# Performance work log

Hardware: AMD Instinct MI355X
Metric: run time of the kernel (lower is better)

## Reference

```python
import math
import jax
import jax.numpy as jnp
import numpy as np

GRID = 12  # distance + 1 for distance-11 surface code


def _ln(x, s, b):
    m = jnp.mean(x, axis=-1, keepdims=True)
    v = jnp.mean((x - m) ** 2, axis=-1, keepdims=True)
    return (x - m) / jnp.sqrt(v + 1e-5) * s + b


def _gelu(x):
    return jax.nn.gelu(x, approximate=False)  # torch F.gelu default = exact erf


def _forward(meas, event, leak, event_leak, bias, pm_w, pm_b, pe_w, pe_b, pl_w, pl_b, pel_w, pel_b,
             stab_emb, cyc_emb, er_ln_s, er_ln_b, er_fc1_w, er_fc1_b, er_fc2_w, er_fc2_b,
             ln1_s, ln1_b, Wb, Wq, bq, Wk, bk, Wv, bv, Wo, bo, ln2_s, ln2_b,
             f1_w, f1_b, f2_w, f2_b, conv_w, conv_b, lnf_s, lnf_b,
             P, sc_w, sc_b, dr_w, dr_b, rb1_w, rb1_b, rb2_w, rb2_b, out_w, out_b,
             stab_ids, cycle_ids):
    B, T, S = meas.shape
    L, Hh, _, da = Wq.shape
    dm = Wv.shape[-1]
    d = P.shape[0]

    # per-head additive attention bias, identical across cycles: (L,B,H,S,S)
    Bp = jnp.einsum('bijd,ldh->lbhij', bias, Wb)
    scale = 1.0 / jnp.sqrt(jnp.asarray(da, meas.dtype))
    pos_emb = stab_emb[stab_ids]  # (S, d)

    def embed(t):
        h = (meas[:, t, :, None] * pm_w + pm_b
             + event[:, t, :, None] * pe_w + pe_b
             + leak[:, t, :, None] * pl_w + pl_b
             + event_leak[:, t, :, None] * pel_w + pel_b
             + pos_emb[None] + cyc_emb[cycle_ids[t]][None, None, :])
        for r in range(er_fc1_w.shape[0]):
            hn = _ln(h, er_ln_s[r], er_ln_b[r])
            h = h + jnp.matmul(_gelu(jnp.matmul(hn, er_fc1_w[r]) + er_fc1_b[r]), er_fc2_w[r]) + er_fc2_b[r]
        return h

    X = jnp.zeros((B, S, d), meas.dtype)
    for t in range(T):  # recurrent application of RNNCore over cycles
        X = (X + embed(t)) / jnp.sqrt(jnp.asarray(2.0, meas.dtype))
        for l in range(L):
            Xn = _ln(X, ln1_s[l], ln1_b[l])
            Q = jnp.einsum('bsd,hde->bhse', Xn, Wq[l]) + bq[l][None, :, None, :]
            Kt = jnp.einsum('bsd,hde->bhse', Xn, Wk[l]) + bk[l][None, :, None, :]
            V = jnp.einsum('bsd,hdm->bhsm', Xn, Wv[l]) + bv[l][None, :, None, :]
            Sc = jnp.einsum('bhqe,bhke->bhqk', Q, Kt) + Bp[l]  # bias added BEFORE 1/sqrt(da)
            A = jax.nn.softmax(Sc * scale, axis=-1)
            O = jnp.einsum('bhqk,bhkm->bhqm', A, V)
            Y = O.transpose(0, 2, 1, 3).reshape(B, S, Hh * dm)
            X = X + jnp.matmul(Y, Wo[l]) + bo[l]
            Xn = _ln(X, ln2_s[l], ln2_b[l])
            Yf = jnp.matmul(Xn, f1_w[l]) + f1_b[l]
            a, g = jnp.split(Yf, 2, axis=-1)
            X = X + jnp.matmul(_gelu(a) * g, f2_w[l]) + f2_b[l]
            # conv block: residual depth-mixing Conv1d(k=3, SAME) over the stabilizer axis
            xc = jnp.transpose(X, (0, 2, 1))  # (B, d, S)
            c = jax.lax.conv_general_dilated(xc, conv_w[l], (1,), 'SAME',
                                             dimension_numbers=('NCH', 'OIH', 'NCH'))
            X = X + _gelu(jnp.transpose(c + conv_b[l][None, :, None], (0, 2, 1)))

    # readout
    Xn = _ln(X, lnf_s, lnf_b)
    pad = jnp.broadcast_to(P, (B, GRID * GRID - S, d))  # empty grid cells filled with P
    grid = jnp.concatenate([Xn, pad], axis=1).reshape(B, GRID, GRID, d).transpose(0, 3, 1, 2)
    x = jax.lax.conv_general_dilated(grid, sc_w, (2, 2), 'VALID',
                                     dimension_numbers=('NCHW', 'OIHW', 'NCHW')) + sc_b[None, :, None, None]
    x = _gelu(x)
    x = jnp.einsum('bdhw,rd->brhw', x, dr_w) + dr_b[None, :, None, None]
    x = _gelu(x)
    x = x.mean(axis=2)  # basis 'z': pool over grid rows -> (B, rd, K)
    Kk = x.shape[2]
    x = x.transpose(0, 2, 1).reshape(B * Kk, -1)
    for r in range(rb1_w.shape[0]):
        x = x + jnp.matmul(_gelu(jnp.matmul(x, rb1_w[r]) + rb1_b[r]), rb2_w[r]) + rb2_b[r]
    logits = (jnp.matmul(x, out_w) + out_b).reshape(B, Kk).mean(axis=1)
    return logits


def setup_inputs() -> dict:
    key = jax.random.key(0)
    ks = iter(jax.random.split(key, 100))

    def rn(shape, s=0.02):
        return (s * jax.random.normal(next(ks), shape)).astype(jnp.float32)

    B, T, S, d = 16, 8, 120, 128
    L, H, da, dm, db = 2, 4, 32, 32, 32
    rd, nrb, ncyc = 48, 16, 32
    z = lambda *sh: jnp.zeros(sh, jnp.float32)
    o = lambda *sh: jnp.ones(sh, jnp.float32)
    inp = {
        'meas': jax.random.uniform(next(ks), (B, T, S), jnp.float32),
        'event': jax.random.uniform(next(ks), (B, T, S), jnp.float32),
        'leak': jax.random.uniform(next(ks), (B, T, S), jnp.float32),
        'event_leak': jax.random.uniform(next(ks), (B, T, S), jnp.float32),
        'bias': rn((B, S, S, db), 0.5),
        'pm_w': rn((d,)), 'pm_b': z(d),
        'pe_w': rn((d,)), 'pe_b': z(d),
        'pl_w': rn((d,)), 'pl_b': z(d),
        'pel_w': rn((d,)), 'pel_b': z(d),
        'stab_emb': rn((S, d)),
        'cyc_emb': rn((ncyc, d)),
        'er_ln_s': o(2, d), 'er_ln_b': z(2, d),
        'er_fc1_w': rn((2, d, d)), 'er_fc1_b': z(2, d),
        'er_fc2_w': rn((2, d, d)), 'er_fc2_b': z(2, d),
        'ln1_s': o(L, d), 'ln1_b': z(L, d),
        'Wb': rn((L, db, H)),
        'Wq': rn((L, H, d, da)), 'bq': z(L, H, da),
        'Wk': rn((L, H, d, da)), 'bk': z(L, H, da),
        'Wv': rn((L, H, d, dm)), 'bv': z(L, H, dm),
        'Wo': rn((L, H * dm, d)), 'bo': z(L, d),
        'ln2_s': o(L, d), 'ln2_b': z(L, d),
        'f1_w': rn((L, d, 4 * d)), 'f1_b': z(L, 4 * d),
        'f2_w': rn((L, 2 * d, d)), 'f2_b': z(L, d),
        'conv_w': rn((L, d, d, 3)), 'conv_b': z(L, d),
        'lnf_s': o(d), 'lnf_b': z(d),
        'P': z(d),
        'sc_w': rn((d, d, 2, 2)), 'sc_b': z(d),
        'dr_w': rn((rd, d)), 'dr_b': z(rd),
        'rb1_w': rn((nrb, rd, rd)), 'rb1_b': z(nrb, rd),
        'rb2_w': rn((nrb, rd, rd)), 'rb2_b': z(nrb, rd),
        'out_w': rn((rd,)), 'out_b': z(),
        'stab_ids': jnp.arange(S, dtype=jnp.int32),
        'cycle_ids': jnp.arange(T, dtype=jnp.int32),
    }
    return inp


def reference(meas, event, leak, event_leak, bias, pm_w, pm_b, pe_w, pe_b, pl_w, pl_b, pel_w, pel_b,
              stab_emb, cyc_emb, er_ln_s, er_ln_b, er_fc1_w, er_fc1_b, er_fc2_w, er_fc2_b,
              ln1_s, ln1_b, Wb, Wq, bq, Wk, bk, Wv, bv, Wo, bo, ln2_s, ln2_b,
              f1_w, f1_b, f2_w, f2_b, conv_w, conv_b, lnf_s, lnf_b,
              P, sc_w, sc_b, dr_w, dr_b, rb1_w, rb1_b, rb2_w, rb2_b, out_w, out_b,
              stab_ids, cycle_ids):
    return _forward(meas, event, leak, event_leak, bias, pm_w, pm_b, pe_w, pe_b, pl_w, pl_b, pel_w, pel_b,
                    stab_emb, cyc_emb, er_ln_s, er_ln_b, er_fc1_w, er_fc1_b, er_fc2_w, er_fc2_b,
                    ln1_s, ln1_b, Wb, Wq, bq, Wk, bk, Wv, bv, Wo, bo, ln2_s, ln2_b,
                    f1_w, f1_b, f2_w, f2_b, conv_w, conv_b, lnf_s, lnf_b,
                    P, sc_w, sc_b, dr_w, dr_b, rb1_w, rb1_b, rb2_w, rb2_b, out_w, out_b,
                    stab_ids, cycle_ids)
```

## Files before the change

kernel.cpp:

```cpp
#include <hip/hip_runtime.h>
#include <math.h>

#define Dm 128
#define Ssz 120
#define Bsz 16
#define Tcy 8
#define Hh 4
#define DA 32
#define Lly 2
#define RT 8
#define NRT ((Bsz*Ssz)/RT)
#define NROW (Bsz*Ssz)

struct KParams {
    const float *meas, *event_, *leak, *event_leak, *bias;
    const float *pm_w, *pm_b, *pe_w, *pe_b, *pl_w, *pl_b, *pel_w, *pel_b;
    const float *stab_emb, *cyc_emb;
    const float *er_ln_s, *er_ln_b, *er_fc1_w, *er_fc1_b, *er_fc2_w, *er_fc2_b;
    const float *ln1_s, *ln1_b, *Wb, *Wq, *bq, *Wk, *bk, *Wv, *bv, *Wo, *bo;
    const float *ln2_s, *ln2_b, *f1_w, *f1_b, *f2_w, *f2_b, *conv_w, *conv_b;
    const float *lnf_s, *lnf_b, *Pp, *sc_w, *sc_b, *dr_w, *dr_b;
    const float *rb1_w, *rb1_b, *rb2_w, *rb2_b, *out_w, *out_b;
    const int *stab_ids, *cycle_ids;
    float *Bp, *Q, *K, *V, *Y2, *cwT, *E;
};

__device__ __forceinline__ float gelu_f(float x) {
    return 0.5f * x * (1.0f + erff(x * 0.70710678118654752f));
}

__device__ __forceinline__ int swz16(int i, int per_b) {
    return ((((i & 7) << 1) | ((i >> 3) & 1)) * per_b) + (i >> 4);
}

__device__ __forceinline__ void ln_rows8(const float (*src)[Dm], float (*dst)[Dm],
                                         const float* sg, const float* bg, int tid) {
    int r = tid >> 6, g = tid & 63;
    float x0 = src[r][g], x1 = src[r][g + 64];
    float s1 = x0 + x1;
#pragma unroll
    for (int off = 32; off; off >>= 1) s1 += __shfl_xor(s1, off);
    float m = s1 * (1.f / 128.f);
    float d0 = x0 - m, d1 = x1 - m;
    float s2 = d0 * d0 + d1 * d1;
#pragma unroll
    for (int off = 32; off; off >>= 1) s2 += __shfl_xor(s2, off);
    float rstd = rsqrtf(s2 * (1.f / 128.f) + 1e-5f);
    dst[r][g]      = d0 * rstd * sg[g]      + bg[g];
    dst[r][g + 64] = d1 * rstd * sg[g + 64] + bg[g + 64];
}

__device__ __forceinline__ void ln32(const float (*src)[Dm], float (*dst)[Dm],
                                     const float* sg, const float* bg, int tid) {
    int r = tid >> 4, g = tid & 15;
    float v[8];
    float s1 = 0.f;
#pragma unroll
    for (int k = 0; k < 8; k++) { v[k] = src[r][g + 16 * k]; s1 += v[k]; }
#pragma unroll
    for (int off = 8; off; off >>= 1) s1 += __shfl_xor(s1, off);
    float m = s1 * (1.f / 128.f);
    float s2 = 0.f;
#pragma unroll
    for (int k = 0; k < 8; k++) { float d = v[k] - m; s2 += d * d; }
#pragma unroll
    for (int off = 8; off; off >>= 1) s2 += __shfl_xor(s2, off);
    float rstd = rsqrtf(s2 * (1.f / 128.f) + 1e-5f);
#pragma unroll
    for (int k = 0; k < 8; k++)
        dst[r][g + 16 * k] = (v[k] - m) * rstd * sg[g + 16 * k] + bg[g + 16 * k];
}

__global__ __launch_bounds__(256) void k_prepcw(KParams p) {
    int idx = blockIdx.x * 256 + threadIdx.x;
    if (idx >= Lly * Dm * 3 * Dm) return;
    int o = idx & 127; int rest = idx >> 7;
    int k = rest % 3; rest /= 3;
    int i = rest & 127; int l = rest >> 7;
    p.cwT[idx] = p.conv_w[((l * Dm + o) * Dm + i) * 3 + k];
}

__global__ __launch_bounds__(128) void k_bias(KParams p) {
    int blk = blockIdx.x;
    int b = blk / Ssz, i = blk % Ssz;
    int j = threadIdx.x;
    if (j >= Ssz) return;
    const float4* br4 = (const float4*)(p.bias + ((size_t)(b * Ssz + i) * Ssz + j) * 32);
    float a[Lly][4];
#pragma unroll
    for (int l = 0; l < Lly; l++)
#pragma unroll
        for (int h = 0; h < 4; h++) a[l][h] = 0.f;
#pragma unroll
    for (int c4 = 0; c4 < 8; c4++) {
        float bv[4]; *(float4*)bv = br4[c4];
#pragma unroll
        for (int u = 0; u < 4; u++) {
#pragma unroll
            for (int l = 0; l < Lly; l++) {
                const float* w = p.Wb + (l * 32 + c4 * 4 + u) * Hh;
                a[l][0] += bv[u] * w[0]; a[l][1] += bv[u] * w[1];
                a[l][2] += bv[u] * w[2]; a[l][3] += bv[u] * w[3];
            }
        }
    }
    size_t hs = (size_t)Ssz * Ssz;
#pragma unroll
    for (int l = 0; l < Lly; l++) {
        size_t base = (((size_t)(l * Bsz + b) * Hh) * Ssz + i) * Ssz + j;
        p.Bp[base] = a[l][0]; p.Bp[base + hs] = a[l][1];
        p.Bp[base + 2 * hs] = a[l][2]; p.Bp[base + 3 * hs] = a[l][3];
    }
}

__global__ __launch_bounds__(512) void k_embed_all(KParams p) {
    __shared__ float h[32][Dm], hn[32][Dm], t1[32][Dm];
    int t = blockIdx.x / 60, tile = blockIdx.x % 60;
    int row0 = tile * 32;
    int tid = threadIdx.x;
    int cid = p.cycle_ids[t];
    for (int idx = tid; idx < 32 * Dm; idx += 512) {
        int r = idx >> 7, j = idx & 127;
        int row = row0 + r;
        int b = row / Ssz, s = row % Ssz;
        int sid = p.stab_ids[s];
        int mi = (b * Tcy + t) * Ssz + s;
        h[r][j] = p.meas[mi] * p.pm_w[j] + p.pm_b[j]
                + p.event_[mi] * p.pe_w[j] + p.pe_b[j]
                + p.leak[mi] * p.pl_w[j] + p.pl_b[j]
                + p.event_leak[mi] * p.pel_w[j] + p.pel_b[j]
                + p.stab_emb[sid * Dm + j] + p.cyc_emb[cid * Dm + j];
    }
    __syncthreads();
    int g2 = tid >> 7, j = tid & 127;
    for (int rbk = 0; rbk < 2; rbk++) {
        ln32(h, hn, p.er_ln_s + rbk * Dm, p.er_ln_b + rbk * Dm, tid);
        __syncthreads();
        const float* W1 = p.er_fc1_w + rbk * Dm * Dm;
        float acc[8];
#pragma unroll
        for (int rr = 0; rr < 8; rr++) acc[rr] = 0.f;
#pragma unroll 2
        for (int i4 = 0; i4 < 32; i4++) {
            float4 xv[8];
#pragma unroll
            for (int rr = 0; rr < 8; rr++) xv[rr] = *(const float4*)&hn[8 * g2 + rr][i4 * 4];
#pragma unroll
            for (int u = 0; u < 4; u++) {
                float w = W1[(i4 * 4 + u) * Dm + j];
#pragma unroll
                for (int rr = 0; rr < 8; rr++) acc[rr] += ((const float*)&xv[rr])[u] * w;
            }
        }
        float b1 = p.er_fc1_b[rbk * Dm + j];
#pragma unroll
        for (int rr = 0; rr < 8; rr++) t1[8 * g2 + rr][j] = gelu_f(acc[rr] + b1);
        __syncthreads();
        const float* W2 = p.er_fc2_w + rbk * Dm * Dm;
#pragma unroll
        for (int rr = 0; rr < 8; rr++) acc[rr] = 0.f;
#pragma unroll 2
        for (int i4 = 0; i4 < 32; i4++) {
            float4 xv[8];
#pragma unroll
            for (int rr = 0; rr < 8; rr++) xv[rr] = *(const float4*)&t1[8 * g2 + rr][i4 * 4];
#pragma unroll
            for (int u = 0; u < 4; u++) {
                float w = W2[(i4 * 4 + u) * Dm + j];
#pragma unroll
                for (int rr = 0; rr < 8; rr++) acc[rr] += ((const float*)&xv[rr])[u] * w;
            }
        }
        float b2 = p.er_fc2_b[rbk * Dm + j];
#pragma unroll
        for (int rr = 0; rr < 8; rr++) h[8 * g2 + rr][j] += acc[rr] + b2;
        __syncthreads();
    }
    for (int idx = tid; idx < 32 * Dm; idx += 512) {
        int r = idx >> 7, jj = idx & 127;
        p.E[((size_t)t * NROW + row0 + r) * Dm + jj] = h[r][jj];
    }
}

__global__ __launch_bounds__(512) void k_a(KParams p, const float* Xprev, float* Xcur,
                                           int l, int t, int doConv) {
    __shared__ float xr[RT + 2][Dm];
    __shared__ float xn[RT][Dm];
    int rb = swz16(blockIdx.x, Ssz / RT);
    int row0 = rb * RT;
    int b = row0 / Ssz, s0 = row0 % Ssz;
    int tid = threadIdx.x;
    const float inv = 0.70710678118654752f;
    int g2 = tid >> 7, j = tid & 127;

    if (doConv) {
        int lconv = l ^ 1;
        {
            float4* xr4 = (float4*)&xr[0][0];
            for (int i = tid; i < (RT + 2) * Dm / 4; i += 512) {
                int rr = i >> 5, c = i & 31;
                int s = s0 + rr - 1;
                float4 v = make_float4(0.f, 0.f, 0.f, 0.f);
                if (s >= 0 && s < Ssz) v = *(const float4*)(Xprev + (b * Ssz + s) * Dm + 4 * c);
                xr4[i] = v;
            }
        }
        __syncthreads();
        const float* CW = p.cwT + (size_t)lconv * Dm * 3 * Dm + j;
        float a0 = 0.f, a1 = 0.f;
#pragma unroll 2
        for (int i4 = 0; i4 < 32; i4++) {
            float4 xv[4];
#pragma unroll
            for (int rr = 0; rr < 4; rr++) xv[rr] = *(const float4*)&xr[2 * g2 + rr][i4 * 4];
#pragma unroll
            for (int u = 0; u < 4; u++) {
                int i = i4 * 4 + u;
                float w0 = CW[(i * 3 + 0) * Dm];
                float w1 = CW[(i * 3 + 1) * Dm];
                float w2 = CW[(i * 3 + 2) * Dm];
                a0 += w0 * ((const float*)&xv[0])[u] + w1 * ((const float*)&xv[1])[u] + w2 * ((const float*)&xv[2])[u];
                a1 += w0 * ((const float*)&xv[1])[u] + w1 * ((const float*)&xv[2])[u] + w2 * ((const float*)&xv[3])[u];
            }
        }
        float cb = p.conv_b[lconv * Dm + j];
        float v0 = xr[2 * g2 + 1][j] + gelu_f(a0 + cb);
        float v1 = xr[2 * g2 + 2][j] + gelu_f(a1 + cb);
        if (l == 0) {
            v0 = (v0 + p.E[((size_t)t * NROW + row0 + 2 * g2) * Dm + j]) * inv;
            v1 = (v1 + p.E[((size_t)t * NROW + row0 + 2 * g2 + 1) * Dm + j]) * inv;
        }
        Xcur[(row0 + 2 * g2) * Dm + j]     = v0;
        Xcur[(row0 + 2 * g2 + 1) * Dm + j] = v1;
        xn[2 * g2][j] = v0; xn[2 * g2 + 1][j] = v1;
    } else {
        float v0 = p.E[(size_t)(row0 + 2 * g2) * Dm + j] * inv;
        float v1 = p.E[(size_t)(row0 + 2 * g2 + 1) * Dm + j] * inv;
        Xcur[(row0 + 2 * g2) * Dm + j]     = v0;
        Xcur[(row0 + 2 * g2 + 1) * Dm + j] = v1;
        xn[2 * g2][j] = v0; xn[2 * g2 + 1][j] = v1;
    }
    __syncthreads();
    ln_rows8(xn, xn, p.ln1_s + l * Dm, p.ln1_b + l * Dm, tid);
    __syncthreads();
    if (tid < 384) {
        int out = tid >> 7, col = tid & 127;
        int h = col >> 5, e = col & 31;
        const float* W = (out == 0 ? p.Wq : out == 1 ? p.Wk : p.Wv)
                       + ((size_t)(l * Hh + h) * Dm) * DA + e;
        const float* bbp = (out == 0 ? p.bq : out == 1 ? p.bk : p.bv) + (l * Hh + h) * DA + e;
        float acc[8];
#pragma unroll
        for (int rr = 0; rr < 8; rr++) acc[rr] = 0.f;
#pragma unroll 2
        for (int i4 = 0; i4 < 32; i4++) {
            float4 xv[8];
#pragma unroll
            for (int rr = 0; rr < 8; rr++) xv[rr] = *(const float4*)&xn[rr][i4 * 4];
#pragma unroll
            for (int u = 0; u < 4; u++) {
                float w = W[(i4 * 4 + u) * DA];
#pragma unroll
                for (int rr = 0; rr < 8; rr++) acc[rr] += ((const float*)&xv[rr])[u] * w;
            }
        }
        float bv = bbp[0];
        if (out == 2) {
            float* vb = p.V + ((size_t)(b * Hh + h) * DA + e) * Ssz + s0;
            *(float4*)vb       = make_float4(acc[0] + bv, acc[1] + bv, acc[2] + bv, acc[3] + bv);
            *(float4*)(vb + 4) = make_float4(acc[4] + bv, acc[5] + bv, acc[6] + bv, acc[7] + bv);
        } else {
            float* dst = (out == 0 ? p.Q : p.K);
            size_t base = ((size_t)(b * Hh + h) * Ssz + s0) * DA + e;
#pragma unroll
            for (int rr = 0; rr < 8; rr++) dst[base + rr * DA] = acc[rr] + bv;
        }
    }
}

struct AttnBufs {
    float4 Kh4[Ssz][8];
    float4 Vt4[DA][32];
    float sc[RT][Ssz];
    float pvp[2][RT][DA];
};
struct FfnBufs {
    float opW[2][RT][Dm];
    float xres[RT][Dm];
    float xn[RT][Dm];
    float yfg[RT][256];
    float yg[RT][256];
};

__global__ __launch_bounds__(512) void k_b(KParams p, float* X, int l) {
    __shared__ union UB { AttnBufs a; FfnBufs f; } u;
    __shared__ float Yt[RT][Dm];
    __shared__ float dn[RT];
    int rb = swz16(blockIdx.x, Ssz / RT);
    int b = rb / (Ssz / RT), qt = rb % (Ssz / RT);
    int q0 = qt * RT;
    int row0 = rb * RT;
    int tid = threadIdx.x;
    const float scale = 0.17677669529663689f;

    for (int h = 0; h < Hh; h++) {
        __syncthreads();
        {
            const float4* K4 = (const float4*)(p.K + ((size_t)(b * Hh + h) * Ssz) * DA);
            const float4* V4 = (const float4*)(p.V + ((size_t)(b * Hh + h) * DA) * Ssz);
            for (int i = tid; i < 960; i += 512) {
                int k = i >> 3, f = i & 7;
                u.a.Kh4[k][f ^ (k & 7)] = K4[i];
                int e = i / 30, s4 = i % 30;
                u.a.Vt4[e][s4 ^ (e & 7)] = V4[i];
            }
        }
        __syncthreads();
        {
            int r = tid >> 6, c0 = tid & 63;
            int c1 = c0 + 64;
            bool v1 = c1 < Ssz;
            int sw = c0 & 7;
            const float* Bpr = p.Bp + (((size_t)(l * Bsz + b) * Hh + h) * Ssz + q0 + r) * Ssz;
            const float4* Q4r = (const float4*)(p.Q + ((size_t)(b * Hh + h) * Ssz + q0 + r) * DA);
            float d0 = 0.f, d1 = 0.f;
#pragma unroll
            for (int e4 = 0; e4 < 8; e4++) {
                float4 qv = Q4r[e4];
                float4 k0 = u.a.Kh4[c0][e4 ^ sw];
                d0 += qv.x * k0.x + qv.y * k0.y + qv.z * k0.z + qv.w * k0.w;
                if (v1) {
                    float4 k1 = u.a.Kh4[c1][e4 ^ sw];
                    d1 += qv.x * k1.x + qv.y * k1.y + qv.z * k1.z + qv.w * k1.w;
                }
            }
            d0 = (d0 + Bpr[c0]) * scale;
            d1 = v1 ? (d1 + Bpr[c1]) * scale : -1e30f;
            float m = fmaxf(d0, d1);
#pragma unroll
            for (int off = 32; off; off >>= 1) m = fmaxf(m, __shfl_xor(m, off));
            float p0 = expf(d0 - m);
            float p1 = v1 ? expf(d1 - m) : 0.f;
            float s = p0 + p1;
#pragma unroll
            for (int off = 32; off; off >>= 1) s += __shfl_xor(s, off);
            u.a.sc[r][c0] = p0;
            if (v1) u.a.sc[r][c1] = p1;
            if (c0 == 0) dn[r] = s;
        }
        __syncthreads();
        {
            int half = tid >> 8, r = (tid >> 5) & 7, m = tid & 31;
            int sw = m & 7;
            int k40 = half * 15;
            float a = 0.f;
#pragma unroll
            for (int k4 = 0; k4 < 15; k4++) {
                float s4v[4];
                *(float4*)s4v = *(const float4*)&u.a.sc[r][(k40 + k4) * 4];
                float4 vv = u.a.Vt4[m][(k40 + k4) ^ sw];
                a += s4v[0] * vv.x + s4v[1] * vv.y + s4v[2] * vv.z + s4v[3] * vv.w;
            }
            u.a.pvp[half][r][m] = a;
        }
        __syncthreads();
        if (tid < 256) {
            int r = tid >> 5, m = tid & 31;
            Yt[r][h * DA + m] = (u.a.pvp[0][r][m] + u.a.pvp[1][r][m]) / dn[r];
        }
    }
    __syncthreads();
    {
        int pp = tid >> 8, g2 = (tid >> 7) & 1, j = tid & 127;
        {
            const float* W = p.Wo + l * Dm * Dm + j;
            float a[4] = {0.f, 0.f, 0.f, 0.f};
            for (int k4 = pp * 16; k4 < pp * 16 + 16; k4++) {
                float4 yv[4];
#pragma unroll
                for (int rr = 0; rr < 4; rr++) yv[rr] = *(const float4*)&Yt[4 * g2 + rr][k4 * 4];
#pragma unroll
                for (int u2 = 0; u2 < 4; u2++) {
                    float w = W[(k4 * 4 + u2) * Dm];
#pragma unroll
                    for (int rr = 0; rr < 4; rr++) a[rr] += ((const float*)&yv[rr])[u2] * w;
                }
            }
#pragma unroll
            for (int rr = 0; rr < 4; rr++) u.f.opW[pp][4 * g2 + rr][j] = a[rr];
        }
        __syncthreads();
        for (int idx = tid; idx < RT * Dm; idx += 512) {
            int r = idx >> 7, j2 = idx & 127;
            float xv = X[(row0 + r) * Dm + j2] + u.f.opW[0][r][j2] + u.f.opW[1][r][j2] + p.bo[l * Dm + j2];
            u.f.xres[r][j2] = xv;
            u.f.xn[r][j2] = xv;
        }
        __syncthreads();
        ln_rows8(u.f.xn, u.f.xn, p.ln2_s + l * Dm, p.ln2_b + l * Dm, tid);
        __syncthreads();
        {
            const float* W1 = p.f1_w + (size_t)l * Dm * 512 + tid;
            float acc[8];
#pragma unroll
            for (int rr = 0; rr < 8; rr++) acc[rr] = 0.f;
#pragma unroll 2
            for (int i4 = 0; i4 < 32; i4++) {
                float4 xv[8];
#pragma unroll
                for (int rr = 0; rr < 8; rr++) xv[rr] = *(const float4*)&u.f.xn[rr][i4 * 4];
#pragma unroll
                for (int u2 = 0; u2 < 4; u2++) {
                    float w = W1[(i4 * 4 + u2) * 512];
#pragma unroll
                    for (int rr = 0; rr < 8; rr++) acc[rr] += ((const float*)&xv[rr])[u2] * w;
                }
            }
            if (tid >= 256) {
#pragma unroll
                for (int rr = 0; rr < 8; rr++) u.f.yfg[rr][tid - 256] = acc[rr];
            }
            __syncthreads();
            if (tid < 256) {
                float b1a = p.f1_b[l * 512 + tid];
                float b1g = p.f1_b[l * 512 + 256 + tid];
#pragma unroll
                for (int rr = 0; rr < 8; rr++)
                    u.f.yg[rr][tid] = gelu_f(acc[rr] + b1a) * (u.f.yfg[rr][tid] + b1g);
            }
        }
        __syncthreads();
        {
            const float* W2 = p.f2_w + (size_t)l * 256 * Dm + j;
            float a[4] = {0.f, 0.f, 0.f, 0.f};
            for (int k4 = pp * 32; k4 < pp * 32 + 32; k4++) {
                float4 yv[4];
#pragma unroll
                for (int rr = 0; rr < 4; rr++) yv[rr] = *(const float4*)&u.f.yg[4 * g2 + rr][k4 * 4];
#pragma unroll
                for (int u2 = 0; u2 < 4; u2++) {
                    float w = W2[(k4 * 4 + u2) * Dm];
#pragma unroll
                    for (int rr = 0; rr < 4; rr++) a[rr] += ((const float*)&yv[rr])[u2] * w;
                }
            }
#pragma unroll
            for (int rr = 0; rr < 4; rr++) u.f.opW[pp][4 * g2 + rr][j] = a[rr];
        }
        __syncthreads();
        for (int idx = tid; idx < RT * Dm; idx += 512) {
            int r = idx >> 7, j2 = idx & 127;
            X[(row0 + r) * Dm + j2] = u.f.xres[r][j2] + u.f.opW[0][r][j2] + u.f.opW[1][r][j2] + p.f2_b[l * Dm + j2];
        }
    }
}

__global__ __launch_bounds__(256) void k_conv(KParams p, const float* Xin, float* Xout, int l) {
    __shared__ float xr[RT + 2][Dm];
    int rb = swz16(blockIdx.x, Ssz / RT);
    int row0 = rb * RT;
    int b = row0 / Ssz, s0 = row0 % Ssz;
    int tid = threadIdx.x;
    {
        float4* xr4 = (float4*)&xr[0][0];
        for (int i = tid; i < (RT + 2) * Dm / 4; i += 256) {
            int rr = i >> 5, c = i & 31;
            int s = s0 + rr - 1;
            float4 v = make_float4(0.f, 0.f, 0.f, 0.f);
            if (s >= 0 && s < Ssz) v = *(const float4*)(Xin + (b * Ssz + s) * Dm + 4 * c);
            xr4[i] = v;
        }
    }
    __syncthreads();
    int g = tid >> 7, j = tid & 127;
    const float* CW = p.cwT + (size_t)l * Dm * 3 * Dm + j;
    float a[4] = {0.f, 0.f, 0.f, 0.f};
#pragma unroll 2
    for (int i4 = 0; i4 < 32; i4++) {
        float4 xv[6];
#pragma unroll
        for (int rr = 0; rr < 6; rr++) xv[rr] = *(const float4*)&xr[4 * g + rr][i4 * 4];
#pragma unroll
        for (int u = 0; u < 4; u++) {
            int i = i4 * 4 + u;
            float w0 = CW[(i * 3 + 0) * Dm];
            float w1 = CW[(i * 3 + 1) * Dm];
            float w2 = CW[(i * 3 + 2) * Dm];
#pragma unroll
            for (int rr = 0; rr < 4; rr++)
                a[rr] += w0 * ((const float*)&xv[rr])[u]
                       + w1 * ((const float*)&xv[rr + 1])[u]
                       + w2 * ((const float*)&xv[rr + 2])[u];
        }
    }
    float cb = p.conv_b[l * Dm + j];
#pragma unroll
    for (int rr = 0; rr < 4; rr++)
        Xout[(row0 + 4 * g + rr) * Dm + j] = xr[4 * g + rr + 1][j] + gelu_f(a[rr] + cb);
}

__global__ __launch_bounds__(128) void k_head(KParams p, const float* X) {
    int blk = swz16(blockIdx.x, 36);
    int b = blk / 36, r2 = blk % 36, oh = r2 / 6, ow = r2 % 6;
    __shared__ float cells[4][Dm];
    __shared__ float sx[Dm];
    int tid = threadIdx.x;
    {
        int c = tid >> 5, lane = tid & 31;
        int cell = (2 * oh + (c >> 1)) * 12 + (2 * ow + (c & 1));
        if (cell < Ssz) {
            const float* Xr = X + (size_t)(b * Ssz + cell) * Dm;
            float v[4];
            float s1 = 0.f;
#pragma unroll
            for (int k = 0; k < 4; k++) { v[k] = Xr[lane + 32 * k]; s1 += v[k]; }
#pragma unroll
            for (int off = 16; off; off >>= 1) s1 += __shfl_xor(s1, off);
            float m = s1 * (1.f / 128.f);
            float s2 = 0.f;
#pragma unroll
            for (int k = 0; k < 4; k++) { float d = v[k] - m; s2 += d * d; }
#pragma unroll
            for (int off = 16; off; off >>= 1) s2 += __shfl_xor(s2, off);
            float rstd = rsqrtf(s2 * (1.f / 128.f) + 1e-5f);
#pragma unroll
            for (int k = 0; k < 4; k++) {
                int jj = lane + 32 * k;
                cells[c][jj] = (v[k] - m) * rstd * p.lnf_s[jj] + p.lnf_b[jj];
            }
        } else {
#pragma unroll
            for (int k = 0; k < 4; k++) cells[c][lane + 32 * k] = p.Pp[lane + 32 * k];
        }
    }
    __syncthreads();
    int j = tid;
    float acc = p.sc_b[j];
    const float* W = p.sc_w + (size_t)j * Dm * 4;
    for (int i = 0; i < Dm; i++) {
        acc += W[i * 4 + 0] * cells[0][i] + W[i * 4 + 1] * cells[1][i]
             + W[i * 4 + 2] * cells[2][i] + W[i * 4 + 3] * cells[3][i];
    }
    sx[j] = gelu_f(acc);
    __syncthreads();
    if (j < 48) {
        float a = p.dr_b[j];
        const float* w = p.dr_w + j * Dm;
        for (int i = 0; i < Dm; i++) a += sx[i] * w[i];
        p.Y2[((b * 6 + ow) * 6 + oh) * 48 + j] = gelu_f(a);
    }
}

__global__ __launch_bounds__(320) void k_rb2(KParams p, float* out) {
    int b = swz16(blockIdx.x, 1);
    __shared__ float x[6][48], t[6][48], red[6];
    int tid = threadIdx.x;
    int ow = tid / 48, j = tid % 48;
    bool act = tid < 288;
    if (act) {
        float s = 0.f;
#pragma unroll
        for (int oh = 0; oh < 6; oh++) s += p.Y2[((b * 6 + ow) * 6 + oh) * 48 + j];
        x[ow][j] = s * (1.f / 6.f);
    }
    __syncthreads();
    for (int r = 0; r < 16; r++) {
        if (act) {
            float a = p.rb1_b[r * 48 + j];
            const float* W = p.rb1_w + (size_t)r * 48 * 48 + j;
            for (int i = 0; i < 48; i++) a += x[ow][i] * W[i * 48];
            t[ow][j] = gelu_f(a);
        }
        __syncthreads();
        if (act) {
            float a = p.rb2_b[r * 48 + j];
            const float* W = p.rb2_w + (size_t)r * 48 * 48 + j;
            for (int i = 0; i < 48; i++) a += t[ow][i] * W[i * 48];
            x[ow][j] += a;
        }
        __syncthreads();
    }
    if (act) t[ow][j] = x[ow][j] * p.out_w[j];
    __syncthreads();
    if (tid < 6) {
        float s = 0.f;
        for (int i = 0; i < 48; i++) s += t[tid][i];
        red[tid] = s;
    }
    __syncthreads();
    if (tid == 0) {
        float s = 0.f;
#pragma unroll
        for (int w = 0; w < 6; w++) s += red[w];
        out[b] = s * (1.f / 6.f) + p.out_b[0];
    }
}

extern "C" void kernel_launch(void* const* d_in, const int* in_sizes, int n_in,
                              void* d_out, int out_size, void* d_ws, size_t ws_size,
                              hipStream_t stream) {
    KParams p;
    p.meas       = (const float*)d_in[0];
    p.event_     = (const float*)d_in[1];
    p.leak       = (const float*)d_in[2];
    p.event_leak = (const float*)d_in[3];
    p.bias       = (const float*)d_in[4];
    p.pm_w  = (const float*)d_in[5];  p.pm_b  = (const float*)d_in[6];
    p.pe_w  = (const float*)d_in[7];  p.pe_b  = (const float*)d_in[8];
    p.pl_w  = (const float*)d_in[9];  p.pl_b  = (const float*)d_in[10];
    p.pel_w = (const float*)d_in[11]; p.pel_b = (const float*)d_in[12];
    p.stab_emb = (const float*)d_in[13];
    p.cyc_emb  = (const float*)d_in[14];
    p.er_ln_s  = (const float*)d_in[15]; p.er_ln_b  = (const float*)d_in[16];
    p.er_fc1_w = (const float*)d_in[17]; p.er_fc1_b = (const float*)d_in[18];
    p.er_fc2_w = (const float*)d_in[19]; p.er_fc2_b = (const float*)d_in[20];
    p.ln1_s = (const float*)d_in[21]; p.ln1_b = (const float*)d_in[22];
    p.Wb = (const float*)d_in[23];
    p.Wq = (const float*)d_in[24]; p.bq = (const float*)d_in[25];
    p.Wk = (const float*)d_in[26]; p.bk = (const float*)d_in[27];
    p.Wv = (const float*)d_in[28]; p.bv = (const float*)d_in[29];
    p.Wo = (const float*)d_in[30]; p.bo = (const float*)d_in[31];
    p.ln2_s = (const float*)d_in[32]; p.ln2_b = (const float*)d_in[33];
    p.f1_w = (const float*)d_in[34]; p.f1_b = (const float*)d_in[35];
    p.f2_w = (const float*)d_in[36]; p.f2_b = (const float*)d_in[37];
    p.conv_w = (const float*)d_in[38]; p.conv_b = (const float*)d_in[39];
    p.lnf_s = (const float*)d_in[40]; p.lnf_b = (const float*)d_in[41];
    p.Pp   = (const float*)d_in[42];
    p.sc_w = (const float*)d_in[43]; p.sc_b = (const float*)d_in[44];
    p.dr_w = (const float*)d_in[45]; p.dr_b = (const float*)d_in[46];
    p.rb1_w = (const float*)d_in[47]; p.rb1_b = (const float*)d_in[48];
    p.rb2_w = (const float*)d_in[49]; p.rb2_b = (const float*)d_in[50];
    p.out_w = (const float*)d_in[51]; p.out_b = (const float*)d_in[52];
    p.stab_ids  = (const int*)d_in[53];
    p.cycle_ids = (const int*)d_in[54];

    float* ws = (float*)d_ws;
    size_t off = 0;
    const size_t BP_SZ  = (size_t)Lly * Bsz * Hh * Ssz * Ssz;
    const size_t QKV_SZ = (size_t)Bsz * Hh * Ssz * DA;
    const size_t X_SZ   = (size_t)Bsz * Ssz * Dm;
    const size_t E_SZ   = (size_t)Tcy * NROW * Dm;
    p.Bp = ws + off; off += BP_SZ;
    p.Q  = ws + off; off += QKV_SZ;
    p.K  = ws + off; off += QKV_SZ;
    p.V  = ws + off; off += QKV_SZ;
    float* X0 = ws + off; off += X_SZ;
    float* X1 = ws + off; off += X_SZ;
    p.Y2  = ws + off; off += (size_t)Bsz * 6 * 6 * 48;
    p.cwT = ws + off; off += (size_t)Lly * Dm * 3 * Dm;
    p.E   = ws + off; off += E_SZ;

    k_prepcw<<<(Lly * Dm * 3 * Dm + 255) / 256, 256, 0, stream>>>(p);
    k_bias<<<Bsz * Ssz, 128, 0, stream>>>(p);
    k_embed_all<<<Tcy * 60, 512, 0, stream>>>(p);

    float* Xbuf[2] = {X0, X1};
    for (int step = 0; step < Tcy * Lly; step++) {
        int t = step >> 1, l = step & 1;
        float* Xcur = Xbuf[step & 1];
        const float* Xprev = (step == 0) ? X0 : Xbuf[(step + 1) & 1];
        k_a<<<NRT, 512, 0, stream>>>(p, Xprev, Xcur, l, t, step > 0 ? 1 : 0);
        k_b<<<NRT, 512, 0, stream>>>(p, Xcur, l);
    }
    k_conv<<<NRT, 256, 0, stream>>>(p, X1, X0, 1);
    k_head<<<Bsz * 36, 128, 0, stream>>>(p, X0);
    k_rb2<<<Bsz, 320, 0, stream>>>(p, (float*)d_out);
}
```

Baseline: 824.2 us.

## Process all attention heads concurrently in shared memory instead of looping per head

K and V for all four heads are staged into shared memory at once. Scores, softmax and the PV product for all heads are then computed in parallel, each by a quarter of the block. This removes the per-head barrier sequence and the split-K partial reduction in PV. In exchange, shared memory use grows to roughly 140KB per block, which limits blocks per CU and may reduce occupancy.

```diff
diff --git a/kernel.cpp b/kernel.cpp
--- a/kernel.cpp
+++ b/kernel.cpp
@@ -279,10 +279,9 @@
 }
 
 struct AttnBufs {
-    float4 Kh4[Ssz][8];
-    float4 Vt4[DA][32];
-    float sc[RT][Ssz];
-    float pvp[2][RT][DA];
+    float4 Kh4[Hh][Ssz][8];
+    float4 Vt4[Hh][DA][32];
+    float sc[Hh][RT][Ssz];
 };
 struct FfnBufs {
     float opW[2][RT][Dm];
@@ -295,7 +294,7 @@
 __global__ __launch_bounds__(512) void k_b(KParams p, float* X, int l) {
     __shared__ union UB { AttnBufs a; FfnBufs f; } u;
     __shared__ float Yt[RT][Dm];
-    __shared__ float dn[RT];
+    __shared__ float dn[Hh][RT];
     int rb = swz16(blockIdx.x, Ssz / RT);
     int b = rb / (Ssz / RT), qt = rb % (Ssz / RT);
     int q0 = qt * RT;
@@ -303,70 +302,72 @@
     int tid = threadIdx.x;
     const float scale = 0.17677669529663689f;
 
-    for (int h = 0; h < Hh; h++) {
-        __syncthreads();
-        {
-            const float4* K4 = (const float4*)(p.K + ((size_t)(b * Hh + h) * Ssz) * DA);
-            const float4* V4 = (const float4*)(p.V + ((size_t)(b * Hh + h) * DA) * Ssz);
-            for (int i = tid; i < 960; i += 512) {
-                int k = i >> 3, f = i & 7;
-                u.a.Kh4[k][f ^ (k & 7)] = K4[i];
-                int e = i / 30, s4 = i % 30;
-                u.a.Vt4[e][s4 ^ (e & 7)] = V4[i];
-            }
-        }
-        __syncthreads();
-        {
-            int r = tid >> 6, c0 = tid & 63;
-            int c1 = c0 + 64;
-            bool v1 = c1 < Ssz;
-            int sw = c0 & 7;
-            const float* Bpr = p.Bp + (((size_t)(l * Bsz + b) * Hh + h) * Ssz + q0 + r) * Ssz;
-            const float4* Q4r = (const float4*)(p.Q + ((size_t)(b * Hh + h) * Ssz + q0 + r) * DA);
-            float d0 = 0.f, d1 = 0.f;
-#pragma unroll
-            for (int e4 = 0; e4 < 8; e4++) {
-                float4 qv = Q4r[e4];
-                float4 k0 = u.a.Kh4[c0][e4 ^ sw];
-                d0 += qv.x * k0.x + qv.y * k0.y + qv.z * k0.z + qv.w * k0.w;
-                if (v1) {
-                    float4 k1 = u.a.Kh4[c1][e4 ^ sw];
-                    d1 += qv.x * k1.x + qv.y * k1.y + qv.z * k1.z + qv.w * k1.w;
+    for (int i = tid; i < Hh * 960; i += 512) {
+        int h = i / 960, i2 = i - h * 960;
+        const float4* K4 = (const float4*)(p.K + ((size_t)(b * Hh + h) * Ssz) * DA);
+        const float4* V4 = (const float4*)(p.V + ((size_t)(b * Hh + h) * DA) * Ssz);
+        int k = i2 >> 3, f = i2 & 7;
+        u.a.Kh4[h][k][f ^ (k & 7)] = K4[i2];
+        int e = i2 / 30, s4 = i2 % 30;
+        u.a.Vt4[h][e][s4 ^ (e & 7)] = V4[i2];
+    }
+    __syncthreads();
+    {
+        int h = tid >> 7, r = (tid >> 4) & 7, l16 = tid & 15;
+        const float4* Q4r = (const float4*)(p.Q + ((size_t)(b * Hh + h) * Ssz + q0 + r) * DA);
+        float4 qv[8];
+#pragma unroll
+        for (int e4 = 0; e4 < 8; e4++) qv[e4] = Q4r[e4];
+        const float* Bpr = p.Bp + (((size_t)(l * Bsz + b) * Hh + h) * Ssz + q0 + r) * Ssz;
+        float d[8];
+#pragma unroll
+        for (int k = 0; k < 8; k++) {
+            int c = l16 + 16 * k;
+            if (c < Ssz) {
+                int sw = c & 7;
+                float dd = 0.f;
+#pragma unroll
+                for (int e4 = 0; e4 < 8; e4++) {
+                    float4 kv = u.a.Kh4[h][c][e4 ^ sw];
+                    dd += qv[e4].x * kv.x + qv[e4].y * kv.y + qv[e4].z * kv.z + qv[e4].w * kv.w;
                 }
-            }
-            d0 = (d0 + Bpr[c0]) * scale;
-            d1 = v1 ? (d1 + Bpr[c1]) * scale : -1e30f;
-            float m = fmaxf(d0, d1);
-#pragma unroll
-            for (int off = 32; off; off >>= 1) m = fmaxf(m, __shfl_xor(m, off));
-            float p0 = expf(d0 - m);
-            float p1 = v1 ? expf(d1 - m) : 0.f;
-            float s = p0 + p1;
-#pragma unroll
-            for (int off = 32; off; off >>= 1) s += __shfl_xor(s, off);
-            u.a.sc[r][c0] = p0;
-            if (v1) u.a.sc[r][c1] = p1;
-            if (c0 == 0) dn[r] = s;
-        }
-        __syncthreads();
-        {
-            int half = tid >> 8, r = (tid >> 5) & 7, m = tid & 31;
-            int sw = m & 7;
-            int k40 = half * 15;
+                d[k] = (dd + Bpr[c]) * scale;
+            } else d[k] = -1e30f;
+        }
+        float m = d[0];
+#pragma unroll
+        for (int k = 1; k < 8; k++) m = fmaxf(m, d[k]);
+#pragma unroll
+        for (int off = 8; off; off >>= 1) m = fmaxf(m, __shfl_xor(m, off));
+        float s = 0.f;
+#pragma unroll
+        for (int k = 0; k < 8; k++) {
+            int c = l16 + 16 * k;
+            if (c < Ssz) {
+                float pv = expf(d[k] - m);
+                u.a.sc[h][r][c] = pv;
+                s += pv;
+            }
+        }
+#pragma unroll
+        for (int off = 8; off; off >>= 1) s += __shfl_xor(s, off);
+        if (l16 == 0) dn[h][r] = s;
+    }
+    __syncthreads();
+    {
+        int h = tid >> 7, r2 = (tid >> 5) & 3, m = tid & 31;
+        int sw = m & 7;
+#pragma unroll
+        for (int rr0 = 0; rr0 < 2; rr0++) {
+            int rr = r2 + rr0 * 4;
             float a = 0.f;
-#pragma unroll
-            for (int k4 = 0; k4 < 15; k4++) {
+            for (int k4 = 0; k4 < 30; k4++) {
                 float s4v[4];
-                *(float4*)s4v = *(const float4*)&u.a.sc[r][(k40 + k4) * 4];
-                float4 vv = u.a.Vt4[m][(k40 + k4) ^ sw];
+                *(float4*)s4v = *(const float4*)&u.a.sc[h][rr][k4 * 4];
+                float4 vv = u.a.Vt4[h][m][k4 ^ sw];
                 a += s4v[0] * vv.x + s4v[1] * vv.y + s4v[2] * vv.z + s4v[3] * vv.w;
             }
-            u.a.pvp[half][r][m] = a;
-        }
-        __syncthreads();
-        if (tid < 256) {
-            int r = tid >> 5, m = tid & 31;
-            Yt[r][h * DA + m] = (u.a.pvp[0][r][m] + u.a.pvp[1][r][m]) / dn[r];
+            Yt[rr][h * DA + m] = a / dn[h][rr];
         }
     }
     __syncthreads();
```

After: 948.0 us. 15.0% more time.

## Fuse final-layer conv into head kernel, removing separate conv launch

Applied to the files above, without the earlier changes.

The last layer's 1D conv plus GELU residual now runs inside k_head. Each head block loads the three neighbouring rows for its four cells and computes the conv only for those cells, then applies the final layernorm. This removes one kernel launch and the round trip of the conv output through global memory. The cost is that each head block does its own 128x384 per-cell conv with strided weight reads and extra shared memory. Neighbouring blocks also reload overlapping rows.

```diff
diff --git a/kernel.cpp b/kernel.cpp
--- a/kernel.cpp
+++ b/kernel.cpp
@@ -455,65 +455,63 @@
     }
 }
 
-__global__ __launch_bounds__(256) void k_conv(KParams p, const float* Xin, float* Xout, int l) {
-    __shared__ float xr[RT + 2][Dm];
-    int rb = swz16(blockIdx.x, Ssz / RT);
-    int row0 = rb * RT;
-    int b = row0 / Ssz, s0 = row0 % Ssz;
-    int tid = threadIdx.x;
-    {
-        float4* xr4 = (float4*)&xr[0][0];
-        for (int i = tid; i < (RT + 2) * Dm / 4; i += 256) {
-            int rr = i >> 5, c = i & 31;
-            int s = s0 + rr - 1;
-            float4 v = make_float4(0.f, 0.f, 0.f, 0.f);
-            if (s >= 0 && s < Ssz) v = *(const float4*)(Xin + (b * Ssz + s) * Dm + 4 * c);
-            xr4[i] = v;
-        }
-    }
-    __syncthreads();
-    int g = tid >> 7, j = tid & 127;
-    const float* CW = p.cwT + (size_t)l * Dm * 3 * Dm + j;
-    float a[4] = {0.f, 0.f, 0.f, 0.f};
-#pragma unroll 2
-    for (int i4 = 0; i4 < 32; i4++) {
-        float4 xv[6];
-#pragma unroll
-        for (int rr = 0; rr < 6; rr++) xv[rr] = *(const float4*)&xr[4 * g + rr][i4 * 4];
-#pragma unroll
-        for (int u = 0; u < 4; u++) {
-            int i = i4 * 4 + u;
-            float w0 = CW[(i * 3 + 0) * Dm];
-            float w1 = CW[(i * 3 + 1) * Dm];
-            float w2 = CW[(i * 3 + 2) * Dm];
-#pragma unroll
-            for (int rr = 0; rr < 4; rr++)
-                a[rr] += w0 * ((const float*)&xv[rr])[u]
-                       + w1 * ((const float*)&xv[rr + 1])[u]
-                       + w2 * ((const float*)&xv[rr + 2])[u];
-        }
-    }
-    float cb = p.conv_b[l * Dm + j];
-#pragma unroll
-    for (int rr = 0; rr < 4; rr++)
-        Xout[(row0 + 4 * g + rr) * Dm + j] = xr[4 * g + rr + 1][j] + gelu_f(a[rr] + cb);
-}
-
 __global__ __launch_bounds__(128) void k_head(KParams p, const float* X) {
     int blk = swz16(blockIdx.x, 36);
     int b = blk / 36, r2 = blk % 36, oh = r2 / 6, ow = r2 % 6;
+    __shared__ float xw[4][3][Dm];
     __shared__ float cells[4][Dm];
     __shared__ float sx[Dm];
     int tid = threadIdx.x;
     {
+        float4* dst = (float4*)&xw[0][0][0];
+        for (int i = tid; i < 4 * 3 * (Dm / 4); i += 128) {
+            int c = i / 96, rem = i % 96, rr = rem / 32, q = rem % 32;
+            int cell = (2 * oh + (c >> 1)) * 12 + (2 * ow + (c & 1));
+            int s = cell - 1 + rr;
+            float4 v = make_float4(0.f, 0.f, 0.f, 0.f);
+            if (cell < Ssz && s >= 0 && s < Ssz)
+                v = *(const float4*)(X + (size_t)(b * Ssz + s) * Dm + 4 * q);
+            dst[i] = v;
+        }
+    }
+    __syncthreads();
+    int j = tid;
+    {
+        const float* CW = p.cwT + (size_t)1 * Dm * 3 * Dm + j;
+        float cb = p.conv_b[1 * Dm + j];
+#pragma unroll
+        for (int c = 0; c < 4; c++) {
+            int cell = (2 * oh + (c >> 1)) * 12 + (2 * ow + (c & 1));
+            if (cell < Ssz) {
+                float acc = 0.f;
+#pragma unroll 2
+                for (int i4 = 0; i4 < 32; i4++) {
+                    float4 x0 = *(const float4*)&xw[c][0][i4 * 4];
+                    float4 x1 = *(const float4*)&xw[c][1][i4 * 4];
+                    float4 x2 = *(const float4*)&xw[c][2][i4 * 4];
+#pragma unroll
+                    for (int u = 0; u < 4; u++) {
+                        int i = i4 * 4 + u;
+                        acc += CW[(i * 3 + 0) * Dm] * ((const float*)&x0)[u]
+                             + CW[(i * 3 + 1) * Dm] * ((const float*)&x1)[u]
+                             + CW[(i * 3 + 2) * Dm] * ((const float*)&x2)[u];
+                    }
+                }
+                cells[c][j] = xw[c][1][j] + gelu_f(acc + cb);
+            } else {
+                cells[c][j] = p.Pp[j];
+            }
+        }
+    }
+    __syncthreads();
+    {
         int c = tid >> 5, lane = tid & 31;
         int cell = (2 * oh + (c >> 1)) * 12 + (2 * ow + (c & 1));
         if (cell < Ssz) {
-            const float* Xr = X + (size_t)(b * Ssz + cell) * Dm;
             float v[4];
             float s1 = 0.f;
 #pragma unroll
-            for (int k = 0; k < 4; k++) { v[k] = Xr[lane + 32 * k]; s1 += v[k]; }
+            for (int k = 0; k < 4; k++) { v[k] = cells[c][lane + 32 * k]; s1 += v[k]; }
 #pragma unroll
             for (int off = 16; off; off >>= 1) s1 += __shfl_xor(s1, off);
             float m = s1 * (1.f / 128.f);
@@ -528,13 +526,9 @@
                 int jj = lane + 32 * k;
                 cells[c][jj] = (v[k] - m) * rstd * p.lnf_s[jj] + p.lnf_b[jj];
             }
-        } else {
-#pragma unroll
-            for (int k = 0; k < 4; k++) cells[c][lane + 32 * k] = p.Pp[lane + 32 * k];
-        }
-    }
-    __syncthreads();
-    int j = tid;
+        }
+    }
+    __syncthreads();
     float acc = p.sc_b[j];
     const float* W = p.sc_w + (size_t)j * Dm * 4;
     for (int i = 0; i < Dm; i++) {
@@ -662,7 +656,6 @@
         k_a<<<NRT, 512, 0, stream>>>(p, Xprev, Xcur, l, t, step > 0 ? 1 : 0);
         k_b<<<NRT, 512, 0, stream>>>(p, Xcur, l);
     }
-    k_conv<<<NRT, 256, 0, stream>>>(p, X1, X0, 1);
-    k_head<<<Bsz * 36, 128, 0, stream>>>(p, X0);
+    k_head<<<Bsz * 36, 128, 0, stream>>>(p, X1);
     k_rb2<<<Bsz, 320, 0, stream>>>(p, (float*)d_out);
 }
```

Measured after the change: 831.1 us. Within noise of the previous version (+0.8%).
